# Optimization experiments

Hardware: AMD Instinct MI355X
Metric: run time of the kernel (lower is better)

Reference implementation:

```python
import jax, jax.numpy as jnp
import numpy as np
from jax import lax

V, D, H, B, S = 30000, 300, 300, 512, 100
DA, WIND1, HOPS, NC = 100, 40, 3, 7


def setup_inputs() -> dict:
    key = jax.random.key(0)
    ks = iter(jax.random.split(key, 64))
    def w(shape, fan_in):
        return jax.random.normal(next(ks), shape, jnp.float32) / np.float32(np.sqrt(fan_in))
    inp = {}
    inp["sents"] = jax.random.randint(next(ks), (B, S), 0, V)
    inp["lengths"] = jax.random.randint(next(ks), (B,), 1, S + 1)
    inp["emb"] = w((V, D), D)
    for d in ("f", "b"):
        inp["lstm_Wih_" + d] = w((4 * H, D), D)
        inp["lstm_Whh_" + d] = w((4 * H, H), H)
        inp["lstm_bih_" + d] = w((4 * H,), H)
        inp["lstm_bhh_" + d] = w((4 * H,), H)
        inp["gru_Wih_" + d] = w((3 * DA, DA), DA)
        inp["gru_Whh_" + d] = w((3 * DA, DA), DA)
        inp["gru_bih_" + d] = w((3 * DA,), DA)
        inp["gru_bhh_" + d] = w((3 * DA,), DA)
    inp["lin1_W"] = w((DA, 2 * H), 2 * H)
    inp["lin1_b"] = w((DA,), 2 * H)
    for nm in ("att_Wr", "att_Ur", "att_W", "att_U"):
        inp[nm] = w((HOPS, DA, DA), DA)
    for nm in ("att_br", "att_bur", "att_bw", "att_bu"):
        inp[nm] = w((HOPS, DA), DA)
    inp["cls_W"] = w((NC, DA), DA)
    inp["cls_b"] = w((NC,), DA)
    return inp


def _lstm_dir(x_tm, m_tm, Wih, Whh, bih, bhh):
    # x_tm: [S,B,D], m_tm: [S,B,1] bool. Masked scan == pack_padded semantics
    xg = jnp.einsum('sbd,gd->sbg', x_tm, Wih) + bih  # precompute input gates [S,B,4H]
    Hh = Whh.shape[1]
    def step(carry, inp):
        h, c = carry
        xgt, mt = inp
        g = xgt + h @ Whh.T + bhh
        i, f, gg, o = jnp.split(g, 4, -1)  # torch LSTM gate order i,f,g,o
        cn = jax.nn.sigmoid(f) * c + jax.nn.sigmoid(i) * jnp.tanh(gg)
        hn = jax.nn.sigmoid(o) * jnp.tanh(cn)
        return (jnp.where(mt, hn, h), jnp.where(mt, cn, c)), jnp.where(mt, hn, 0.0)
    init = (jnp.zeros((x_tm.shape[1], Hh), x_tm.dtype), jnp.zeros((x_tm.shape[1], Hh), x_tm.dtype))
    _, out = lax.scan(step, init, (xg, m_tm))
    return out


def _gru_dir(x_tm, Wih, Whh, bih, bhh):
    xg = jnp.einsum('sbd,gd->sbg', x_tm, Wih) + bih  # [S,B,3H]
    Hh = Whh.shape[1]
    def step(h, xgt):
        hg = h @ Whh.T + bhh
        xr, xz, xn = jnp.split(xgt, 3, -1)
        hr, hz, hn = jnp.split(hg, 3, -1)
        r = jax.nn.sigmoid(xr + hr)
        z = jax.nn.sigmoid(xz + hz)
        n = jnp.tanh(xn + r * hn)
        h2 = (1.0 - z) * n + z * h
        return h2, h2
    _, out = lax.scan(step, jnp.zeros((x_tm.shape[1], Hh), x_tm.dtype), xg)
    return out


def _attgru(mem_tm, gates_tm, Wr, br, Ur, bur, W, bw, U, bu):
    # mem_tm: [W,B-1,100], gates_tm: [W,B-1,1]; AttnGRUCell recurrence
    cr = jnp.einsum('sbd,hd->sbh', mem_tm, Wr) + br
    cw = jnp.einsum('sbd,hd->sbh', mem_tm, W) + bw
    def step(h, inp):
        crt, cwt, g = inp
        r = jax.nn.sigmoid(crt + h @ Ur.T + bur)
        ht = jnp.tanh(cwt + r * (h @ U.T + bu))
        return g * ht + (1.0 - g) * h, None
    h0 = jnp.zeros((mem_tm.shape[1], Wr.shape[0]), mem_tm.dtype)
    h, _ = lax.scan(step, h0, (cr, cw, gates_tm))
    return h  # [B-1,100]


def reference(sents, lengths, emb,
              lstm_Wih_f, lstm_Whh_f, lstm_bih_f, lstm_bhh_f,
              lstm_Wih_b, lstm_Whh_b, lstm_bih_b, lstm_bhh_b,
              lin1_W, lin1_b,
              gru_Wih_f, gru_Whh_f, gru_bih_f, gru_bhh_f,
              gru_Wih_b, gru_Whh_b, gru_bih_b, gru_bhh_b,
              att_Wr, att_br, att_Ur, att_bur, att_W, att_bw, att_U, att_bu,
              cls_W, cls_b):
    we = emb[sents]  # [B,S,D]
    mask = jnp.arange(S)[None, :] < lengths[:, None]  # [B,S]
    x_tm = we.transpose(1, 0, 2)
    m_tm = mask.T[:, :, None]
    out_f = _lstm_dir(x_tm, m_tm, lstm_Wih_f, lstm_Whh_f, lstm_bih_f, lstm_bhh_f)
    out_b = jnp.flip(_lstm_dir(jnp.flip(x_tm, 0), jnp.flip(m_tm, 0),
                               lstm_Wih_b, lstm_Whh_b, lstm_bih_b, lstm_bhh_b), 0)
    w_gru = jnp.concatenate([out_f, out_b], -1).transpose(1, 0, 2)  # [B,S,2H], 0 at pads
    maxpl = jnp.max(w_gru, axis=1)
    s_utt = jnp.tanh(maxpl @ lin1_W.T + lin1_b)  # [B,100]; dropout = eval identity
    # context window: slot j of query i holds utterance i-WIND1+j (zero-padded front)
    idx = jnp.arange(1, B)[:, None] - WIND1 + jnp.arange(WIND1)[None, :]  # [B-1,W]
    valid = idx >= 0
    bt = s_utt[jnp.clip(idx, 0)] * valid[..., None].astype(s_utt.dtype)  # [B-1,W,100]
    bt_tm = bt.transpose(1, 0, 2)  # [W,B-1,100]
    mem_f = _gru_dir(bt_tm, gru_Wih_f, gru_Whh_f, gru_bih_f, gru_bhh_f)
    mem_b = jnp.flip(_gru_dir(jnp.flip(bt_tm, 0), gru_Wih_b, gru_Whh_b, gru_bih_b, gru_bhh_b), 0)
    mem_tm = bt_tm + mem_f + mem_b  # fusion: input + fwd + bwd GRU states
    mem_bank = mem_tm.transpose(1, 0, 2)  # [B-1,W,100]
    eps = s_utt[1:][:, None, :]  # query [B-1,1,100]
    attn_ws = []
    for hop in range(HOPS):
        attn = jnp.einsum('bqd,bkd->bqk', eps, mem_bank)  # [B-1,1,W]
        attn = jnp.where(valid[:, None, :], attn, -1e10)
        scores = jax.nn.softmax(attn, -1)
        gates_tm = scores[:, 0, :].T[:, :, None]  # [W,B-1,1]
        h = _attgru(mem_tm, gates_tm, att_Wr[hop], att_br[hop], att_Ur[hop], att_bur[hop],
                    att_W[hop], att_bw[hop], att_U[hop], att_bu[hop])
        eps = eps + h[:, None, :]
        attn_ws.append(scores[:, 0, :])
    s_cont = jnp.concatenate([s_utt[:1], eps[:, 0, :]], 0)  # [B,100]
    pred = jax.nn.log_softmax(s_cont @ cls_W.T + cls_b, -1)  # [B,NC]
    return pred, jnp.stack(attn_ws)  # attn weights [HOPS,B-1,W]
```

## Files before the change

### kernel.cpp

```cpp
#include <hip/hip_runtime.h>
#include <cstdint>
#include <cstddef>

typedef unsigned short u16;
typedef unsigned int   u32;
typedef unsigned long long u64;

#define S_LEN 100
#define B_SZ  512
#define H_LS  300
#define NHOP  3
#define NC_   7
#define BM1   511
#define NBD4  120

using bf16x8 = __attribute__((ext_vector_type(8))) short;
using f32x4  = __attribute__((ext_vector_type(4))) float;

__device__ __forceinline__ float u2f(u16 u) {
  union { u32 i; float f; } x; x.i = ((u32)u) << 16; return x.f;
}
__device__ __forceinline__ u16 f2u(float f) {
  u32 bits = __float_as_uint(f);
  bits += 0x7fffu + ((bits >> 16) & 1u);
  return (u16)(bits >> 16);
}
__device__ __forceinline__ float sigm(float x) { return 1.0f / (1.0f + expf(-x)); }

__global__ void detect_k(const u32* __restrict__ raw, int* __restrict__ flag) {
  __shared__ int cnt;
  if (threadIdx.x == 0) cnt = 0;
  __syncthreads();
  u32 w = raw[threadIdx.x];
  u32 lo = w & 0xFFFFu;
  int e = (int)((lo >> 7) & 0xFF);
  int pl = (lo == 0u || (e >= 0x70 && e <= 0x8E)) ? 1 : 0;
  atomicAdd(&cnt, pl);
  __syncthreads();
  if (threadIdx.x == 0) *flag = (cnt >= 192) ? 1 : 0;
}

#define NF_NSEG 28
#define NF_TOT  1748007
struct NormFArgs { const void* src[NF_NSEG]; const int* flag; float* dst; };

__global__ __launch_bounds__(256) void norm_f32(NormFArgs a) {
  const int P[NF_NSEG + 1] = {
    0,360000,720000,1080000,1440000,1441200,1442400,1443600,
    1444800,1474800,1504800,1505100,1505400,1535400,1565400,1565700,
    1566000,1626000,1626100,1656100,1686100,1716100,1746100,1746400,
    1746700,1747000,1747300,1748000,1748007};
  int fl = *a.flag;
  int stride = gridDim.x * 256;
  for (int i = blockIdx.x * 256 + threadIdx.x; i < NF_TOT; i += stride) {
    int s = 0;
    while (i >= P[s + 1]) ++s;
    int k = i - P[s];
    float v = fl ? u2f(((const u16*)a.src[s])[k]) : ((const float*)a.src[s])[k];
    a.dst[i] = v;
  }
}
#define AF_LWIH_F 0
#define AF_LWHH_F 360000
#define AF_LWIH_B 720000
#define AF_LWHH_B 1080000
#define AF_LBIH_F 1440000
#define AF_LBHH_F 1441200
#define AF_LBIH_B 1442400
#define AF_LBHH_B 1443600
#define AF_GWIH_F 1444800
#define AF_GWHH_F 1474800
#define AF_GBIH_F 1504800
#define AF_GBHH_F 1505100
#define AF_GWIH_B 1505400
#define AF_GWHH_B 1535400
#define AF_GBIH_B 1565400
#define AF_GBHH_B 1565700
#define AF_LIN1W  1566000
#define AF_LIN1B  1626000
#define AF_ATTWR  1626100
#define AF_ATTUR  1656100
#define AF_ATTW   1686100
#define AF_ATTU   1716100
#define AF_ATTBR  1746100
#define AF_ATTBUR 1746400
#define AF_ATTBW  1746700
#define AF_ATTBU  1747000
#define AF_CLSW   1747300
#define AF_CLSB   1748000

__global__ void transp_k(const float* __restrict__ allf, float* __restrict__ wt) {
  int idx = blockIdx.x * 256 + threadIdx.x;
  if (idx >= 120000) return;
  int seg = idx / 10000;
  int rem = idx - seg * 10000;
  int k = rem / 100, j = rem - (rem / 100) * 100;
  int srcbase;
  if (seg < 3)      srcbase = AF_GWHH_F + seg * 10000;
  else if (seg < 6) srcbase = AF_GWHH_B + (seg - 3) * 10000;
  else if (seg < 9) srcbase = AF_ATTUR + (seg - 6) * 10000;
  else              srcbase = AF_ATTU  + (seg - 9) * 10000;
  wt[seg * 10000 + k * 100 + j] = allf[srcbase + j * 100 + k];
}

__global__ void tr_lstm2(const float* __restrict__ allf, u16* __restrict__ wL2,
                         float* __restrict__ bsum) {
  int idx = blockIdx.x * 256 + threadIdx.x;
  if (idx < 1536000) {
    int dir = idx / 768000;
    int rem = idx - dir * 768000;
    int c = rem / 640, kp = rem - (rem / 640) * 640;
    int j = c >> 2, g = c & 3;
    float v = 0.f;
    if (kp < 320) {
      if (kp < 300)
        v = allf[(dir ? AF_LWIH_B : AF_LWIH_F) + (g * 300 + j) * 300 + kp];
    } else {
      int k2 = kp - 320;
      if (k2 < 300)
        v = allf[(dir ? AF_LWHH_B : AF_LWHH_F) + (g * 300 + j) * 300 + k2];
    }
    wL2[idx] = f2u(v);
  } else if (idx < 1538400) {
    int i2 = idx - 1536000;
    int dir = i2 / 1200, gj = i2 - (i2 / 1200) * 1200;
    bsum[i2] = allf[(dir ? AF_LBIH_B : AF_LBIH_F) + gj]
             + allf[(dir ? AF_LBHH_B : AF_LBHH_F) + gj];
  }
}

__global__ __launch_bounds__(256) void xgat2(const int* __restrict__ sents,
                                             const void* __restrict__ emb,
                                             const int* __restrict__ flag,
                                             u16* __restrict__ xallR) {
  __shared__ int toks[64];
  int tid = threadIdx.x;
  int r0 = blockIdx.x * 64, t = blockIdx.y;
  int fl = *flag;
  if (tid < 64) toks[tid] = sents[(r0 + tid) * S_LEN + t];
  __syncthreads();
  for (int idx = tid; idx < 64 * 320; idx += 256) {
    int r = idx / 320, k = idx - (idx / 320) * 320;
    u16 v = 0;
    if (k < 300) {
      size_t si = (size_t)toks[r] * 300 + k;
      v = fl ? ((const u16*)emb)[si] : f2u(((const float*)emb)[si]);
    }
    xallR[((size_t)t * 512 + r0 + r) * 320 + k] = v;
  }
}

struct Lstm9Args {
  const int* lens;
  const u16* xallR;
  const u16* wL2;
  const float* bsum;
  float* hbufR;
  float* maxb;
  int* cnt;
};

__global__ __launch_bounds__(512, 1) void lstm9(Lstm9Args a) {
  __shared__ u16   WLh[80 * 640];
  __shared__ float Gs[64 * 85];
  const int tid = threadIdx.x;
  const int r0  = blockIdx.x * 64;
  const int ct  = blockIdx.y;
  const int dir = blockIdx.z;

  {
    const u64* wsrc = (const u64*)(a.wL2 + (size_t)dir * 768000 + (size_t)ct * 80 * 640);
    for (int i = tid; i < 80 * 160; i += 512) {
      int cc = i / 160, kw = i - (i / 160) * 160;
      u64 v = wsrc[(size_t)cc * 160 + kw];
      *(u64*)((char*)WLh + cc * 1280 + ((kw * 8) ^ ((cc & 7) << 4))) = v;
    }
  }

  const int w  = tid >> 6;
  const int rf = w & 3;
  const int kh = w >> 2;
  const int l  = tid & 63;
  const int lr = l & 15;
  const int aq = l >> 4;
  const int arow = r0 + rf * 16 + lr;

  float cq[3] = {0.f, 0.f, 0.f}, hq[3] = {0.f, 0.f, 0.f};
  float mxv[3] = {-INFINITY, -INFINITY, -INFINITY};
  float bsv[3][4];
  int lenv[3];
  #pragma unroll
  for (int i = 0; i < 3; ++i) {
    int idx = tid + i * 512;
    if (idx < 1280) {
      int r = idx / 20, jj = idx - (idx / 20) * 20;
      int j = ct * 20 + jj;
      lenv[i] = a.lens[r0 + r];
      #pragma unroll
      for (int g = 0; g < 4; ++g) bsv[i][g] = a.bsum[dir * 1200 + g * 300 + j];
    } else {
      lenv[i] = 0;
      bsv[i][0] = bsv[i][1] = bsv[i][2] = bsv[i][3] = 0.f;
    }
  }

  int* cptr = a.cnt + dir * 32;
  int* fptr = a.cnt + dir * 32 + 16;
  __syncthreads();

  for (int s = 0; s < S_LEN; ++s) {
    const int tt  = dir ? (S_LEN - 1 - s) : s;
    const int cur = s & 1, nxt = cur ^ 1;

    f32x4 acc0 = {0,0,0,0}, acc1 = {0,0,0,0}, acc2 = {0,0,0,0},
          acc3 = {0,0,0,0}, acc4 = {0,0,0,0};

    if (kh == 0) {
      const u16* xrow = a.xallR + ((size_t)tt * 512 + arow) * 320 + aq * 8;
      bf16x8 Af = *(const bf16x8*)(xrow);
      #pragma unroll
      for (int ks = 0; ks < 10; ++ks) {
        bf16x8 An = (ks < 9) ? *(const bf16x8*)(xrow + (ks + 1) * 32) : Af;
        #pragma unroll
        for (int cf = 0; cf < 5; ++cf) {
          int cc = cf * 16 + lr;
          bf16x8 Bf = *(const bf16x8*)((const char*)WLh + cc * 1280 +
                                       ((ks * 64 + aq * 16) ^ ((cc & 7) << 4)));
          f32x4& ac = (cf == 0) ? acc0 : (cf == 1) ? acc1 : (cf == 2) ? acc2
                    : (cf == 3) ? acc3 : acc4;
          ac = __builtin_amdgcn_mfma_f32_16x16x32_bf16(Af, Bf, ac, 0, 0, 0);
        }
        Af = An;
      }
    } else {
      const float* hrow = a.hbufR + (((size_t)cur * 2 + dir) * 512 + arow) * 320 + aq * 8;
      float4 h0 = *(const float4*)hrow;
      float4 h1 = *(const float4*)(hrow + 4);
      #pragma unroll
      for (int ks = 0; ks < 10; ++ks) {
        float4 n0, n1;
        if (ks < 9) {
          n0 = *(const float4*)(hrow + (ks + 1) * 32);
          n1 = *(const float4*)(hrow + (ks + 1) * 32 + 4);
        }
        union { u32 u[4]; bf16x8 v; } pk;
        pk.u[0] = ((u32)f2u(h0.y) << 16) | (u32)f2u(h0.x);
        pk.u[1] = ((u32)f2u(h0.w) << 16) | (u32)f2u(h0.z);
        pk.u[2] = ((u32)f2u(h1.y) << 16) | (u32)f2u(h1.x);
        pk.u[3] = ((u32)f2u(h1.w) << 16) | (u32)f2u(h1.z);
        bf16x8 Af = pk.v;
        #pragma unroll
        for (int cf = 0; cf < 5; ++cf) {
          int cc = cf * 16 + lr;
          bf16x8 Bf = *(const bf16x8*)((const char*)WLh + cc * 1280 +
                                       (((ks + 10) * 64 + aq * 16) ^ ((cc & 7) << 4)));
          f32x4& ac = (cf == 0) ? acc0 : (cf == 1) ? acc1 : (cf == 2) ? acc2
                    : (cf == 3) ? acc3 : acc4;
          ac = __builtin_amdgcn_mfma_f32_16x16x32_bf16(Af, Bf, ac, 0, 0, 0);
        }
        if (ks < 9) { h0 = n0; h1 = n1; }
      }
    }

    if (kh == 0) {
      #pragma unroll
      for (int rr = 0; rr < 4; ++rr) {
        int gr = (rf * 16 + aq * 4 + rr) * 85;
        Gs[gr + 0 * 16 + lr] = acc0[rr];
        Gs[gr + 1 * 16 + lr] = acc1[rr];
        Gs[gr + 2 * 16 + lr] = acc2[rr];
        Gs[gr + 3 * 16 + lr] = acc3[rr];
        Gs[gr + 4 * 16 + lr] = acc4[rr];
      }
    }
    __syncthreads();
    if (kh == 1) {
      #pragma unroll
      for (int rr = 0; rr < 4; ++rr) {
        int gr = (rf * 16 + aq * 4 + rr) * 85;
        Gs[gr + 0 * 16 + lr] += acc0[rr];
        Gs[gr + 1 * 16 + lr] += acc1[rr];
        Gs[gr + 2 * 16 + lr] += acc2[rr];
        Gs[gr + 3 * 16 + lr] += acc3[rr];
        Gs[gr + 4 * 16 + lr] += acc4[rr];
      }
    }
    __syncthreads();

    #pragma unroll
    for (int i = 0; i < 3; ++i) {
      int idx = tid + i * 512;
      if (idx < 1280) {
        int r = idx / 20, jj = idx - (idx / 20) * 20;
        bool m = tt < lenv[i];
        if (m) {
          float gi = Gs[r * 85 + jj * 4 + 0] + bsv[i][0];
          float gf = Gs[r * 85 + jj * 4 + 1] + bsv[i][1];
          float gg = Gs[r * 85 + jj * 4 + 2] + bsv[i][2];
          float go = Gs[r * 85 + jj * 4 + 3] + bsv[i][3];
          cq[i] = sigm(gf) * cq[i] + sigm(gi) * tanhf(gg);
          hq[i] = sigm(go) * tanhf(cq[i]);
          mxv[i] = fmaxf(mxv[i], hq[i]);
        } else {
          mxv[i] = fmaxf(mxv[i], 0.f);
        }
        a.hbufR[(((size_t)nxt * 2 + dir) * 512 + r0 + r) * 320 + ct * 20 + jj] = hq[i];
      }
    }

    __syncthreads();
    if (tid == 0) {
      __threadfence();
      int old = __hip_atomic_fetch_add(cptr, 1, __ATOMIC_ACQ_REL, __HIP_MEMORY_SCOPE_AGENT);
      if (old == NBD4 * (s + 1) - 1) {
        __hip_atomic_store(fptr, s + 1, __ATOMIC_RELEASE, __HIP_MEMORY_SCOPE_AGENT);
      } else {
        while (__hip_atomic_load(fptr, __ATOMIC_ACQUIRE, __HIP_MEMORY_SCOPE_AGENT) < s + 1)
          __builtin_amdgcn_s_sleep(2);
      }
      __threadfence();
    }
    __syncthreads();
  }

  #pragma unroll
  for (int i = 0; i < 3; ++i) {
    int idx = tid + i * 512;
    if (idx < 1280) {
      int r = idx / 20, jj = idx - (idx / 20) * 20;
      a.maxb[(size_t)(r0 + r) * 600 + dir * 300 + ct * 20 + jj] = mxv[i];
    }
  }
}

__global__ __launch_bounds__(128) void sutt_k(const float* __restrict__ maxb,
                                              const float* __restrict__ W,
                                              const float* __restrict__ bb,
                                              float* __restrict__ sutt) {
  int b = blockIdx.x, tid = threadIdx.x;
  __shared__ float mx[600];
  for (int i = tid; i < 600; i += 128) mx[i] = maxb[b * 600 + i];
  __syncthreads();
  if (tid < 100) {
    float acc = bb[tid];
    const float* wr = W + tid * 600;
    for (int k = 0; k < 600; ++k) acc += mx[k] * wr[k];
    sutt[b * 100 + tid] = tanhf(acc);
  }
}

__global__ __launch_bounds__(256) void gxg3(const float* __restrict__ sutt,
                                            const float* __restrict__ Wf, const float* __restrict__ bf_,
                                            const float* __restrict__ Wb, const float* __restrict__ bb_,
                                            float* __restrict__ xg) {
  __shared__ float bts[32][101];
  int tid = threadIdx.x;
  int rt = blockIdx.x * 32, t = blockIdx.y, dir = blockIdx.z;
  int tin = dir ? (39 - t) : t;
  for (int idx = tid; idx < 3200; idx += 256) {
    int r = idx / 100, k = idx - r * 100, row = rt + r;
    float v = 0.f;
    if (row < BM1) {
      int srow = row + 1 - 40 + tin;
      if (srow >= 0) v = sutt[srow * 100 + k];
    }
    bts[r][k] = v;
  }
  __syncthreads();
  const float* Wm = dir ? Wb : Wf;
  const float* bm = dir ? bb_ : bf_;
  for (int o = tid; o < 9600; o += 256) {
    int r = o & 31, g = o >> 5;
    float acc = bm[g];
    const float* wr = Wm + g * 100;
    const float* br = bts[r];
    for (int k = 0; k < 100; ++k) acc += br[k] * wr[k];
    int row = rt + r;
    if (row < BM1) xg[(((size_t)dir * 40 + t) * BM1 + row) * 300 + g] = acc;
  }
}

struct Gru4Args {
  const float* wt;
  const float* bhh[2];
  const float* xg;
  float* memf; float* memb;
};

__global__ __launch_bounds__(512) void gru4(Gru4Args a) {
  __shared__ float WT[30000];
  __shared__ float hl[2][4][104];
  int tid = threadIdx.x, rt = blockIdx.x * 4, dir = blockIdx.y;
  const float* src = a.wt + dir * 30000;
  for (int i = tid; i < 30000; i += 512) WT[i] = src[i];
  for (int i = tid; i < 832; i += 512) ((float*)hl)[i] = 0.f;
  int r = tid / 100, j = tid - r * 100;
  int row = rt + r;
  bool act = (tid < 400) && (row < BM1);
  const float* bhh = a.bhh[dir];
  float xr = 0.f, xz = 0.f, xn = 0.f;
  if (act) {
    size_t xb = ((size_t)(dir * 40) * BM1 + row) * 300;
    xr = a.xg[xb + j]; xz = a.xg[xb + 100 + j]; xn = a.xg[xb + 200 + j];
  }
  float hprev = 0.f;
  __syncthreads();
  for (int t = 0; t < 40; ++t) {
    int nxt = (t + 1) & 1, cur = t & 1;
    float xr2 = 0.f, xz2 = 0.f, xn2 = 0.f;
    if (act && t < 39) {
      size_t xb = ((size_t)(dir * 40 + t + 1) * BM1 + row) * 300;
      xr2 = a.xg[xb + j]; xz2 = a.xg[xb + 100 + j]; xn2 = a.xg[xb + 200 + j];
    }
    float v = 0.f;
    if (act) {
      float hr = bhh[j], hz = bhh[100 + j], hn = bhh[200 + j];
      const float* w0 = WT + j;
      const float* hrow = hl[cur][r];
      for (int k = 0; k < 100; ++k) {
        float hv = hrow[k];
        hr += hv * w0[k * 100];
        hz += hv * w0[10000 + k * 100];
        hn += hv * w0[20000 + k * 100];
      }
      float rg_ = sigm(xr + hr), zg = sigm(xz + hz);
      float ng = tanhf(xn + rg_ * hn);
      v = (1.f - zg) * ng + zg * hprev;
      int tin = dir ? (39 - t) : t;
      (dir ? a.memb : a.memf)[((size_t)tin * BM1 + row) * 100 + j] = v;
    }
    if (tid < 400) hl[nxt][r][j] = v;
    hprev = v;
    __syncthreads();
    xr = xr2; xz = xz2; xn = xn2;
  }
}

__global__ void memcomb(const float* __restrict__ memf, const float* __restrict__ memb,
                        const float* __restrict__ sutt, float* __restrict__ memm) {
  int idx = blockIdx.x * 256 + threadIdx.x;
  if (idx >= 40 * BM1 * 100) return;
  int j = idx % 100; int rem = idx / 100; int row = rem % BM1; int t = rem / BM1;
  float v = memf[idx] + memb[idx];
  int sidx = row + 1 - 40 + t;
  if (sidx >= 0) v += sutt[sidx * 100 + j];
  memm[idx] = v;
}

__global__ void epsinit(const float* __restrict__ sutt, float* __restrict__ eps) {
  int idx = blockIdx.x * 256 + threadIdx.x;
  if (idx < BM1 * 100) eps[idx] = sutt[idx + 100];
}

__global__ __launch_bounds__(64) void attnsc(const float* __restrict__ eps,
                                             const float* __restrict__ memm,
                                             float* __restrict__ gatesw,
                                             float* __restrict__ outat) {
  int row = blockIdx.x, k = threadIdx.x;
  __shared__ float el[100];
  for (int i = k; i < 100; i += 64) el[i] = eps[row * 100 + i];
  __syncthreads();
  float val = -INFINITY;
  if (k < 40) {
    if (row + 1 - 40 + k >= 0) {
      const float* mrow = memm + ((size_t)k * BM1 + row) * 100;
      float s = 0.f;
      for (int d = 0; d < 100; ++d) s += el[d] * mrow[d];
      val = s;
    } else val = -1e10f;
  }
  float mx = val;
  for (int off = 32; off > 0; off >>= 1) mx = fmaxf(mx, __shfl_xor(mx, off));
  float ex = (k < 40) ? expf(val - mx) : 0.f;
  float sm = ex;
  for (int off = 32; off > 0; off >>= 1) sm += __shfl_xor(sm, off);
  if (k < 40) {
    float sc = ex / sm;
    gatesw[k * BM1 + row] = sc;
    outat[row * 40 + k] = sc;
  }
}

__global__ __launch_bounds__(256) void crcw3(const float* __restrict__ memm,
                                             const float* __restrict__ Wr, const float* __restrict__ br,
                                             const float* __restrict__ Ww, const float* __restrict__ bw,
                                             float* __restrict__ crb, float* __restrict__ cwb) {
  __shared__ float ml[32][101];
  int tid = threadIdx.x;
  int rt = blockIdx.x * 32, t = blockIdx.y, which = blockIdx.z;
  for (int idx = tid; idx < 3200; idx += 256) {
    int r = idx / 100, k = idx - r * 100; int row = rt + r;
    ml[r][k] = (row < BM1) ? memm[((size_t)t * BM1 + row) * 100 + k] : 0.f;
  }
  __syncthreads();
  const float* Wm = which ? Ww : Wr;
  const float* bm = which ? bw : br;
  float* ob = which ? cwb : crb;
  for (int o = tid; o < 3200; o += 256) {
    int r = o & 31, hh = o >> 5;
    float acc = bm[hh];
    const float* wr = Wm + hh * 100;
    for (int k = 0; k < 100; ++k) acc += ml[r][k] * wr[k];
    int row = rt + r;
    if (row < BM1) ob[((size_t)t * BM1 + row) * 100 + hh] = acc;
  }
}

struct Att4Args {
  const float* urT; const float* uT;
  const float* bur; const float* bu;
  const float* crb; const float* cwb;
  const float* gatesw; float* eps;
};

__global__ __launch_bounds__(512) void attscan4(Att4Args a) {
  __shared__ float UrT[10000];
  __shared__ float UT[10000];
  __shared__ float hl[2][4][104];
  int tid = threadIdx.x, rt = blockIdx.x * 4;
  for (int i = tid; i < 10000; i += 512) { UrT[i] = a.urT[i]; UT[i] = a.uT[i]; }
  for (int i = tid; i < 832; i += 512) ((float*)hl)[i] = 0.f;
  int r = tid / 100, j = tid - r * 100;
  int row = rt + r;
  bool act = (tid < 400) && (row < BM1);
  float cr = 0.f, cw = 0.f, gw = 0.f;
  if (act) {
    size_t ix = (size_t)row * 100 + j;
    cr = a.crb[ix]; cw = a.cwb[ix]; gw = a.gatesw[row];
  }
  float hprev = 0.f;
  __syncthreads();
  for (int t = 0; t < 40; ++t) {
    int nxt = (t + 1) & 1, cur = t & 1;
    float cr2 = 0.f, cw2 = 0.f, gw2 = 0.f;
    if (act && t < 39) {
      size_t ix = ((size_t)(t + 1) * BM1 + row) * 100 + j;
      cr2 = a.crb[ix]; cw2 = a.cwb[ix]; gw2 = a.gatesw[(t + 1) * BM1 + row];
    }
    float v = 0.f;
    if (act) {
      float hr = a.bur[j], hu = a.bu[j];
      const float* hrow = hl[cur][r];
      for (int k = 0; k < 100; ++k) {
        float hv = hrow[k];
        hr += hv * UrT[k * 100 + j];
        hu += hv * UT[k * 100 + j];
      }
      float rg_ = sigm(cr + hr);
      float ht = tanhf(cw + rg_ * hu);
      v = gw * ht + (1.f - gw) * hprev;
    }
    if (tid < 400) hl[nxt][r][j] = v;
    hprev = v;
    __syncthreads();
    cr = cr2; cw = cw2; gw = gw2;
  }
  if (act) a.eps[(size_t)row * 100 + j] += hprev;
}

__global__ __launch_bounds__(64) void cls_k(const float* __restrict__ sutt,
                                            const float* __restrict__ eps,
                                            const float* __restrict__ cW, const float* __restrict__ cb,
                                            float* __restrict__ outp) {
  int b = blockIdx.x, j = threadIdx.x;
  __shared__ float sl[100];
  for (int i = j; i < 100; i += 64) sl[i] = (b == 0) ? sutt[i] : eps[(b - 1) * 100 + i];
  __syncthreads();
  float lg = -INFINITY;
  if (j < 7) {
    lg = cb[j];
    const float* wr = cW + j * 100;
    for (int k = 0; k < 100; ++k) lg += sl[k] * wr[k];
  }
  float mx = lg;
  for (int off = 32; off > 0; off >>= 1) mx = fmaxf(mx, __shfl_xor(mx, off));
  float ex = (j < 7) ? expf(lg - mx) : 0.f;
  float sm = ex;
  for (int off = 32; off > 0; off >>= 1) sm += __shfl_xor(sm, off);
  if (j < 7) outp[b * 7 + j] = lg - mx - logf(sm);
}

extern "C" void kernel_launch(void* const* d_in, const int* in_sizes, int n_in,
                              void* d_out, int out_size, void* d_ws, size_t ws_size,
                              hipStream_t stream) {
  (void)n_in; (void)out_size; (void)ws_size;

  bool sigOrder = (in_sizes[7] == 360000);

  const void *p_sents, *p_lens, *p_emb;
  const void *p_lWih_f, *p_lWhh_f, *p_lbih_f, *p_lbhh_f;
  const void *p_lWih_b, *p_lWhh_b, *p_lbih_b, *p_lbhh_b;
  const void *p_gWih_f, *p_gWhh_f, *p_gbih_f, *p_gbhh_f;
  const void *p_gWih_b, *p_gWhh_b, *p_gbih_b, *p_gbhh_b;
  const void *p_lin1W, *p_lin1b;
  const void *p_attWr, *p_attUr, *p_attW, *p_attU;
  const void *p_attbr, *p_attbur, *p_attbw, *p_attbu;
  const void *p_clsW, *p_clsb;

  p_sents = d_in[0]; p_lens = d_in[1]; p_emb = d_in[2];
  p_lWih_f = d_in[3]; p_lWhh_f = d_in[4]; p_lbih_f = d_in[5]; p_lbhh_f = d_in[6];
  if (sigOrder) {
    p_lWih_b = d_in[7];  p_lWhh_b = d_in[8];  p_lbih_b = d_in[9];  p_lbhh_b = d_in[10];
    p_lin1W  = d_in[11]; p_lin1b  = d_in[12];
    p_gWih_f = d_in[13]; p_gWhh_f = d_in[14]; p_gbih_f = d_in[15]; p_gbhh_f = d_in[16];
    p_gWih_b = d_in[17]; p_gWhh_b = d_in[18]; p_gbih_b = d_in[19]; p_gbhh_b = d_in[20];
    p_attWr  = d_in[21]; p_attbr  = d_in[22]; p_attUr  = d_in[23]; p_attbur = d_in[24];
    p_attW   = d_in[25]; p_attbw  = d_in[26]; p_attU   = d_in[27]; p_attbu  = d_in[28];
    p_clsW   = d_in[29]; p_clsb   = d_in[30];
  } else {
    p_gWih_f = d_in[7];  p_gWhh_f = d_in[8];  p_gbih_f = d_in[9];  p_gbhh_f = d_in[10];
    p_lWih_b = d_in[11]; p_lWhh_b = d_in[12]; p_lbih_b = d_in[13]; p_lbhh_b = d_in[14];
    p_gWih_b = d_in[15]; p_gWhh_b = d_in[16]; p_gbih_b = d_in[17]; p_gbhh_b = d_in[18];
    p_lin1W  = d_in[19]; p_lin1b  = d_in[20];
    p_attWr  = d_in[21]; p_attUr  = d_in[22]; p_attW   = d_in[23]; p_attU   = d_in[24];
    p_attbr  = d_in[25]; p_attbur = d_in[26]; p_attbw  = d_in[27]; p_attbu  = d_in[28];
    p_clsW   = d_in[29]; p_clsb   = d_in[30];
  }

  char* wp = (char*)d_ws;
  auto carve = [&](size_t bytes) {
    char* p = wp;
    wp += (bytes + 255) & ~(size_t)255;
    return p;
  };
  int*   flag  = (int*)  carve(256);
  int*   cnt   = (int*)  carve(256);
  float* allf  = (float*)carve((size_t)NF_TOT * 4);
  float* wt    = (float*)carve((size_t)120000 * 4);
  u16*   wL2   = (u16*)  carve((size_t)1536000 * 2);
  float* bsum  = (float*)carve((size_t)2400 * 4);
  float* hbufR = (float*)carve((size_t)2 * 2 * 512 * 320 * 4);
  float* maxb  = (float*)carve((size_t)B_SZ * 600 * 4);
  float* sutt  = (float*)carve((size_t)B_SZ * 100 * 4);
  size_t xg_sz   = (size_t)2 * 40 * BM1 * 300 * 4;
  size_t memf_sz = (size_t)40 * BM1 * 100 * 4;
  char*  big   = carve(xg_sz + 2 * memf_sz);
  u16*   xallR = (u16*)big;
  float* xg    = (float*)big;
  float* memf  = (float*)(big + xg_sz);
  float* memb  = (float*)(big + xg_sz + memf_sz);
  float* memm  = (float*)carve(memf_sz);
  float* gatesw= (float*)carve((size_t)40 * BM1 * 4);
  float* eps   = (float*)carve((size_t)BM1 * 100 * 4);
  float* crb   = xg;
  float* cwb   = xg + (size_t)40 * BM1 * 100;

  float* out_pred = (float*)d_out;
  float* out_attn = out_pred + (size_t)B_SZ * NC_;

  detect_k<<<1, 256, 0, stream>>>((const u32*)p_emb, flag);

  NormFArgs nf;
  {
    const void* srcs[NF_NSEG] = {
      p_lWih_f, p_lWhh_f, p_lWih_b, p_lWhh_b,
      p_lbih_f, p_lbhh_f, p_lbih_b, p_lbhh_b,
      p_gWih_f, p_gWhh_f, p_gbih_f, p_gbhh_f,
      p_gWih_b, p_gWhh_b, p_gbih_b, p_gbhh_b,
      p_lin1W,  p_lin1b,
      p_attWr,  p_attUr,  p_attW,   p_attU,
      p_attbr,  p_attbur, p_attbw,  p_attbu,
      p_clsW,   p_clsb };
    for (int i = 0; i < NF_NSEG; ++i) nf.src[i] = srcs[i];
    nf.flag = flag; nf.dst = allf;
  }
  norm_f32<<<2048, 256, 0, stream>>>(nf);
  transp_k<<<(120000 + 255) / 256, 256, 0, stream>>>(allf, wt);
  tr_lstm2<<<(1538400 + 255) / 256, 256, 0, stream>>>(allf, wL2, bsum);
  xgat2<<<dim3(8, 100), 256, 0, stream>>>((const int*)p_sents, p_emb, flag, xallR);

  hipMemsetAsync(cnt, 0, 256, stream);
  hipMemsetAsync(hbufR, 0, (size_t)2 * 2 * 512 * 320 * 4, stream);

  Lstm9Args la;
  la.lens = (const int*)p_lens;
  la.xallR = xallR; la.wL2 = wL2; la.bsum = bsum;
  la.hbufR = hbufR; la.maxb = maxb; la.cnt = cnt;
  lstm9<<<dim3(8, 15, 2), 512, 0, stream>>>(la);

  sutt_k<<<512, 128, 0, stream>>>(maxb, allf + AF_LIN1W, allf + AF_LIN1B, sutt);

  gxg3<<<dim3(16, 40, 2), 256, 0, stream>>>(sutt,
      allf + AF_GWIH_F, allf + AF_GBIH_F,
      allf + AF_GWIH_B, allf + AF_GBIH_B, xg);

  Gru4Args ga;
  ga.wt = wt;
  ga.bhh[0] = allf + AF_GBHH_F; ga.bhh[1] = allf + AF_GBHH_B;
  ga.xg = xg; ga.memf = memf; ga.memb = memb;
  gru4<<<dim3(128, 2), 512, 0, stream>>>(ga);

  memcomb<<<(40 * BM1 * 100 + 255) / 256, 256, 0, stream>>>(memf, memb, sutt, memm);
  epsinit<<<(BM1 * 100 + 255) / 256, 256, 0, stream>>>(sutt, eps);

  for (int hop = 0; hop < NHOP; ++hop) {
    attnsc<<<BM1, 64, 0, stream>>>(eps, memm, gatesw, out_attn + (size_t)hop * BM1 * 40);
    crcw3<<<dim3(16, 40, 2), 256, 0, stream>>>(memm,
        allf + AF_ATTWR + hop * 10000, allf + AF_ATTBR + hop * 100,
        allf + AF_ATTW  + hop * 10000, allf + AF_ATTBW + hop * 100, crb, cwb);
    Att4Args aa;
    aa.urT = wt + 60000 + hop * 10000;
    aa.uT  = wt + 90000 + hop * 10000;
    aa.bur = allf + AF_ATTBUR + hop * 100;
    aa.bu  = allf + AF_ATTBU  + hop * 100;
    aa.crb = crb; aa.cwb = cwb;
    aa.gatesw = gatesw; aa.eps = eps;
    attscan4<<<128, 512, 0, stream>>>(aa);
  }

  cls_k<<<512, 64, 0, stream>>>(sutt, eps, allf + AF_CLSW, allf + AF_CLSB, out_pred);
}
```

Before: 3.941 ms.

## Scope LSTM grid barrier to row-block groups and split warps by output columns

The per-timestep grid barrier now synchronizes only the 15 column-tile blocks that share a 64-row batch slice and direction, instead of all 120 blocks of a direction. Each group gets its own counter, padded onto a separate cache line. The warp split also changes from the K dimension (input half vs hidden half, which needed a second shared-memory reduction pass and an extra block barrier) to output column fragments (3 and 2), so each warp does both K halves and writes its gates directly. The cost is an uneven 3/2 MFMA load across warp halves and a shorter spin-wait sleep.

After: 3.716 ms. -5.7%, faster.

```diff
diff --git a/kernel.cpp b/kernel.cpp
--- a/kernel.cpp
+++ b/kernel.cpp
@@ -12,7 +12,7 @@
 #define NHOP  3
 #define NC_   7
 #define BM1   511
-#define NBD4  120
+#define GRPSZ 15
 
 using bf16x8 = __attribute__((ext_vector_type(8))) short;
 using f32x4  = __attribute__((ext_vector_type(4))) float;
@@ -150,7 +150,7 @@
   }
 }
 
-struct Lstm9Args {
+struct Lstm10Args {
   const int* lens;
   const u16* xallR;
   const u16* wL2;
@@ -160,7 +160,7 @@
   int* cnt;
 };
 
-__global__ __launch_bounds__(512, 1) void lstm9(Lstm9Args a) {
+__global__ __launch_bounds__(512, 1) void lstm10(Lstm10Args a) {
   __shared__ u16   WLh[80 * 640];
   __shared__ float Gs[64 * 85];
   const int tid = threadIdx.x;
@@ -179,7 +179,9 @@
 
   const int w  = tid >> 6;
   const int rf = w & 3;
-  const int kh = w >> 2;
+  const int ch = w >> 2;
+  const int cf0 = ch ? 3 : 0;
+  const int ncf = ch ? 2 : 3;
   const int l  = tid & 63;
   const int lr = l & 15;
   const int aq = l >> 4;
@@ -204,35 +206,38 @@
     }
   }
 
-  int* cptr = a.cnt + dir * 32;
-  int* fptr = a.cnt + dir * 32 + 16;
+  const int gi = dir * 8 + blockIdx.x;
+  int* cptr = a.cnt + gi * 64;
+  int* fptr = a.cnt + gi * 64 + 16;
   __syncthreads();
 
   for (int s = 0; s < S_LEN; ++s) {
     const int tt  = dir ? (S_LEN - 1 - s) : s;
     const int cur = s & 1, nxt = cur ^ 1;
 
-    f32x4 acc0 = {0,0,0,0}, acc1 = {0,0,0,0}, acc2 = {0,0,0,0},
-          acc3 = {0,0,0,0}, acc4 = {0,0,0,0};
-
-    if (kh == 0) {
+    f32x4 acc[3];
+    #pragma unroll
+    for (int i = 0; i < 3; ++i) acc[i] = (f32x4){0, 0, 0, 0};
+
+    {
       const u16* xrow = a.xallR + ((size_t)tt * 512 + arow) * 320 + aq * 8;
       bf16x8 Af = *(const bf16x8*)(xrow);
       #pragma unroll
       for (int ks = 0; ks < 10; ++ks) {
         bf16x8 An = (ks < 9) ? *(const bf16x8*)(xrow + (ks + 1) * 32) : Af;
         #pragma unroll
-        for (int cf = 0; cf < 5; ++cf) {
-          int cc = cf * 16 + lr;
-          bf16x8 Bf = *(const bf16x8*)((const char*)WLh + cc * 1280 +
-                                       ((ks * 64 + aq * 16) ^ ((cc & 7) << 4)));
-          f32x4& ac = (cf == 0) ? acc0 : (cf == 1) ? acc1 : (cf == 2) ? acc2
-                    : (cf == 3) ? acc3 : acc4;
-          ac = __builtin_amdgcn_mfma_f32_16x16x32_bf16(Af, Bf, ac, 0, 0, 0);
+        for (int i = 0; i < 3; ++i) {
+          if (i < ncf) {
+            int cc = (cf0 + i) * 16 + lr;
+            bf16x8 Bf = *(const bf16x8*)((const char*)WLh + cc * 1280 +
+                                         ((ks * 64 + aq * 16) ^ ((cc & 7) << 4)));
+            acc[i] = __builtin_amdgcn_mfma_f32_16x16x32_bf16(Af, Bf, acc[i], 0, 0, 0);
+          }
         }
         Af = An;
       }
-    } else {
+    }
+    {
       const float* hrow = a.hbufR + (((size_t)cur * 2 + dir) * 512 + arow) * 320 + aq * 8;
       float4 h0 = *(const float4*)hrow;
       float4 h1 = *(const float4*)(hrow + 4);
@@ -250,39 +255,24 @@
         pk.u[3] = ((u32)f2u(h1.w) << 16) | (u32)f2u(h1.z);
         bf16x8 Af = pk.v;
         #pragma unroll
-        for (int cf = 0; cf < 5; ++cf) {
-          int cc = cf * 16 + lr;
-          bf16x8 Bf = *(const bf16x8*)((const char*)WLh + cc * 1280 +
-                                       (((ks + 10) * 64 + aq * 16) ^ ((cc & 7) << 4)));
-          f32x4& ac = (cf == 0) ? acc0 : (cf == 1) ? acc1 : (cf == 2) ? acc2
-                    : (cf == 3) ? acc3 : acc4;
-          ac = __builtin_amdgcn_mfma_f32_16x16x32_bf16(Af, Bf, ac, 0, 0, 0);
+        for (int i = 0; i < 3; ++i) {
+          if (i < ncf) {
+            int cc = (cf0 + i) * 16 + lr;
+            bf16x8 Bf = *(const bf16x8*)((const char*)WLh + cc * 1280 +
+                                         (((ks + 10) * 64 + aq * 16) ^ ((cc & 7) << 4)));
+            acc[i] = __builtin_amdgcn_mfma_f32_16x16x32_bf16(Af, Bf, acc[i], 0, 0, 0);
+          }
         }
         if (ks < 9) { h0 = n0; h1 = n1; }
       }
     }
 
-    if (kh == 0) {
+    #pragma unroll
+    for (int rr = 0; rr < 4; ++rr) {
+      int gr = (rf * 16 + aq * 4 + rr) * 85;
       #pragma unroll
-      for (int rr = 0; rr < 4; ++rr) {
-        int gr = (rf * 16 + aq * 4 + rr) * 85;
-        Gs[gr + 0 * 16 + lr] = acc0[rr];
-        Gs[gr + 1 * 16 + lr] = acc1[rr];
-        Gs[gr + 2 * 16 + lr] = acc2[rr];
-        Gs[gr + 3 * 16 + lr] = acc3[rr];
-        Gs[gr + 4 * 16 + lr] = acc4[rr];
-      }
-    }
-    __syncthreads();
-    if (kh == 1) {
-      #pragma unroll
-      for (int rr = 0; rr < 4; ++rr) {
-        int gr = (rf * 16 + aq * 4 + rr) * 85;
-        Gs[gr + 0 * 16 + lr] += acc0[rr];
-        Gs[gr + 1 * 16 + lr] += acc1[rr];
-        Gs[gr + 2 * 16 + lr] += acc2[rr];
-        Gs[gr + 3 * 16 + lr] += acc3[rr];
-        Gs[gr + 4 * 16 + lr] += acc4[rr];
+      for (int i = 0; i < 3; ++i) {
+        if (i < ncf) Gs[gr + (cf0 + i) * 16 + lr] = acc[i][rr];
       }
     }
     __syncthreads();
@@ -294,11 +284,11 @@
         int r = idx / 20, jj = idx - (idx / 20) * 20;
         bool m = tt < lenv[i];
         if (m) {
-          float gi = Gs[r * 85 + jj * 4 + 0] + bsv[i][0];
-          float gf = Gs[r * 85 + jj * 4 + 1] + bsv[i][1];
-          float gg = Gs[r * 85 + jj * 4 + 2] + bsv[i][2];
-          float go = Gs[r * 85 + jj * 4 + 3] + bsv[i][3];
-          cq[i] = sigm(gf) * cq[i] + sigm(gi) * tanhf(gg);
+          float gi_ = Gs[r * 85 + jj * 4 + 0] + bsv[i][0];
+          float gf  = Gs[r * 85 + jj * 4 + 1] + bsv[i][1];
+          float gg  = Gs[r * 85 + jj * 4 + 2] + bsv[i][2];
+          float go  = Gs[r * 85 + jj * 4 + 3] + bsv[i][3];
+          cq[i] = sigm(gf) * cq[i] + sigm(gi_) * tanhf(gg);
           hq[i] = sigm(go) * tanhf(cq[i]);
           mxv[i] = fmaxf(mxv[i], hq[i]);
         } else {
@@ -312,11 +302,11 @@
     if (tid == 0) {
       __threadfence();
       int old = __hip_atomic_fetch_add(cptr, 1, __ATOMIC_ACQ_REL, __HIP_MEMORY_SCOPE_AGENT);
-      if (old == NBD4 * (s + 1) - 1) {
+      if (old == GRPSZ * (s + 1) - 1) {
         __hip_atomic_store(fptr, s + 1, __ATOMIC_RELEASE, __HIP_MEMORY_SCOPE_AGENT);
       } else {
         while (__hip_atomic_load(fptr, __ATOMIC_ACQUIRE, __HIP_MEMORY_SCOPE_AGENT) < s + 1)
-          __builtin_amdgcn_s_sleep(2);
+          __builtin_amdgcn_s_sleep(1);
       }
       __threadfence();
     }
@@ -624,7 +614,7 @@
     return p;
   };
   int*   flag  = (int*)  carve(256);
-  int*   cnt   = (int*)  carve(256);
+  int*   cnt   = (int*)  carve(4096);
   float* allf  = (float*)carve((size_t)NF_TOT * 4);
   float* wt    = (float*)carve((size_t)120000 * 4);
   u16*   wL2   = (u16*)  carve((size_t)1536000 * 2);
@@ -669,14 +659,14 @@
   tr_lstm2<<<(1538400 + 255) / 256, 256, 0, stream>>>(allf, wL2, bsum);
   xgat2<<<dim3(8, 100), 256, 0, stream>>>((const int*)p_sents, p_emb, flag, xallR);
 
-  hipMemsetAsync(cnt, 0, 256, stream);
+  hipMemsetAsync(cnt, 0, 4096, stream);
   hipMemsetAsync(hbufR, 0, (size_t)2 * 2 * 512 * 320 * 4, stream);
 
-  Lstm9Args la;
+  Lstm10Args la;
   la.lens = (const int*)p_lens;
   la.xallR = xallR; la.wL2 = wL2; la.bsum = bsum;
   la.hbufR = hbufR; la.maxb = maxb; la.cnt = cnt;
-  lstm9<<<dim3(8, 15, 2), 512, 0, stream>>>(la);
+  lstm10<<<dim3(8, 15, 2), 512, 0, stream>>>(la);
 
   sutt_k<<<512, 128, 0, stream>>>(maxb, allf + AF_LIN1W, allf + AF_LIN1B, sutt);
 
```
